# Performance work log

Measured on AMD Instinct MI355X. Metric: run time of the kernel, lower is better.

## Reference

```python
import jax, jax.numpy as jnp
import numpy as np

B, L, H = 4, 200, 225   # batch, seq_len, hidden (=15*15)
V = 221                 # input_dim + 1 (padding_idx=0)
EPS = 1e-5


def _bn(x, g, b):
    # training-mode batchnorm over (N, spatial), channel axis = 1
    red = (0,) + tuple(range(2, x.ndim))
    m = jnp.mean(x, red, keepdims=True)
    v = jnp.var(x, red, keepdims=True)
    shp = [1] * x.ndim
    shp[1] = -1
    return (x - m) / jnp.sqrt(v + EPS) * g.reshape(shp) + b.reshape(shp)


def _conv3(x, w, sd):
    return jax.lax.conv_general_dilated(
        x, w, (sd, 1, 1), [(1, 1)] * 3,
        dimension_numbers=('NCDHW', 'OIDHW', 'NCDHW'))


def _conv2(x, w):
    return jax.lax.conv_general_dilated(
        x, w, (1, 1), [(1, 1)] * 2,
        dimension_numbers=('NCHW', 'OIHW', 'NCHW'))


def setup_inputs():
    key = jax.random.key(0)
    ks = jax.random.split(key, 16)

    def he(k, shape, fan_in):
        return jax.random.normal(k, shape, jnp.float32) * (2.0 / fan_in) ** 0.5

    emb = he(ks[0], (V, H), H).at[0].set(0.0)  # padding_idx=0 row zeroed
    w3a = he(ks[1], (4, 1, 3, 3, 3), 1 * 27)
    w3b = he(ks[2], (8, 4, 3, 3, 3), 4 * 27)
    w3c = he(ks[3], (4, 8, 3, 3, 3), 8 * 27)
    w3d = he(ks[4], (1, 4, 3, 3, 3), 4 * 27)
    w2 = he(ks[5], (5, 25, 25, 3, 3), 25 * 9)  # 5 residual conv2d blocks
    fc1_w = he(ks[6], (200, 450), 450)
    fc1_b = jnp.zeros((200,), jnp.float32)
    fc2_w = he(ks[7], (1, 200), 200)
    fc2_b = jnp.zeros((1,), jnp.float32)
    x = jax.random.randint(ks[8], (B, L), 0, V)
    return dict(
        x=x, emb=emb,
        w3a=w3a, g3a=jnp.ones(4), b3a=jnp.zeros(4),
        w3b=w3b, g3b=jnp.ones(8), b3b=jnp.zeros(8),
        w3c=w3c, g3c=jnp.ones(4), b3c=jnp.zeros(4),
        w3d=w3d, g3d=jnp.ones(1), b3d=jnp.zeros(1),
        w2=w2, g2=jnp.ones((5, 25)), b2=jnp.zeros((5, 25)),
        fc1_w=fc1_w, fc1_b=fc1_b, fc2_w=fc2_w, fc2_b=fc2_b)


def reference(x, emb, w3a, g3a, b3a, w3b, g3b, b3b, w3c, g3c, b3c,
              w3d, g3d, b3d, w2, g2, b2, fc1_w, fc1_b, fc2_w, fc2_b):
    e = emb[x]                                  # [B,L,225]
    img = e.reshape(B, L, 15, 15)
    # vectorized replacement of python double-loop causal mask/pad construction:
    # c3d[b,i,t] = img[b,t] if t <= i else 0
    mask = jnp.tril(jnp.ones((L, L), e.dtype))
    c3d = (img[:, None] * mask[None, :, :, None, None]).reshape(B * L, 1, L, 15, 15)

    h = jax.nn.relu(_bn(_conv3(c3d, w3a, 1), g3a, b3a))   # [N,4,200,15,15]
    h = jax.nn.relu(_bn(_conv3(h, w3b, 2), g3b, b3b))     # [N,8,100,15,15]
    h = jax.nn.relu(_bn(_conv3(h, w3c, 2), g3c, b3c))     # [N,4,50,15,15]
    h = jax.nn.relu(_bn(_conv3(h, w3d, 2), g3d, b3d))     # [N,1,25,15,15]

    z = h[:, 0]                                 # squeeze -> [N,25,15,15]
    for i in range(5):
        z = z + jax.nn.relu(_bn(_conv2(z, w2[i]), g2[i], b2[i]))

    # AdaptiveAvgPool3d((1,15,15)) on [N,1,25,15,15] == mean over depth 25
    pooled = jnp.mean(z, axis=1).reshape(B * L, 225)
    feat = jnp.concatenate([pooled, e.reshape(B * L, 225)], axis=1)  # [N,450]
    hfc = jnp.tanh(feat @ fc1_w.T + fc1_b)
    return jax.nn.sigmoid(hfc @ fc2_w.T + fc2_b)  # [N,1]
```

## Files before the change

### kernel.cpp

```cpp
#include <hip/hip_runtime.h>
#include <math.h>

#define DEV __device__ __forceinline__

constexpr int B = 4, L = 200, SP = 225;
constexpr int C1 = 4, D1 = 200;
constexpr int C2N = 8, D2 = 100;
constexpr int C3N = 4, D3 = 50;
constexpr int D4 = 25;
constexpr float EPS = 1e-5f;

constexpr size_t OFF_F1  = 0;
constexpr size_t OFF_E2  = OFF_F1  + 720000;
constexpr size_t OFF_E1  = OFF_E2  + 720000;
constexpr size_t OFF_SS1 = OFF_E1  + 720000;
constexpr size_t OFF_PAR = OFF_SS1 + 19200;
constexpr size_t OFF_F2  = OFF_PAR + 1024;
constexpr size_t OFF_C2  = OFF_F2  + 720000;
constexpr size_t OFF_T2  = OFF_C2  + 1800;
constexpr size_t OFF_SS2F= OFF_T2  + 2880000;
constexpr size_t OFF_SS2T= OFF_SS2F+ 6400;
constexpr size_t OFF_SS2C= OFF_SS2T+ 51200;
constexpr size_t OFF_F3  = OFF_SS2C+ 16;
constexpr size_t OFF_C3  = OFF_F3  + 180000;
constexpr size_t OFF_T3  = OFF_C3  + 900;
constexpr size_t OFF_SS3F= OFF_T3  + 1440000;
constexpr size_t OFF_SS3T= OFF_SS3F+ 1600;
constexpr size_t OFF_SS3C= OFF_SS3T+ 12800;
constexpr size_t OFF_F4  = OFF_SS3C+ 8;
constexpr size_t OFF_C4  = OFF_F4  + 22500;
constexpr size_t OFF_T4  = OFF_C4  + 225;
constexpr size_t OFF_SS4F= OFF_T4  + 360000;
constexpr size_t OFF_SS4T= OFF_SS4F+ 200;
constexpr size_t OFF_SS4C= OFF_SS4T+ 3200;
constexpr size_t OFF_Z   = OFF_SS4C+ 2;
constexpr size_t OFF_CB  = OFF_Z   + 4500000;
constexpr size_t OFF_P2D = OFF_CB  + 4500000;
constexpr size_t WS_FLOATS = OFF_P2D + 40000;


DEV float waveRed(float v) {
    #pragma unroll
    for (int m = 32; m; m >>= 1) v += __shfl_xor(v, m, 64);
    return v;
}
DEV double blockSumD(double v, double* red) {
    int tid = threadIdx.x;
    red[tid] = v; __syncthreads();
    for (int s = 128; s > 0; s >>= 1) { if (tid < s) red[tid] += red[tid + s]; __syncthreads(); }
    double r = red[0]; __syncthreads(); return r;
}
DEV float conv9(const float* S, const float* w, int y, int x) {
    float a = 0.f;
    for (int ky = 0; ky < 3; ky++) { int yy = y + ky - 1; if (yy < 0 || yy >= 15) continue;
        for (int kx = 0; kx < 3; kx++) { int xx = x + kx - 1; if (xx < 0 || xx >= 15) continue;
            a += w[ky * 3 + kx] * S[yy * 15 + xx]; } }
    return a;
}
DEV void gather9(const float* Sp, int y, int x, float* s9) {
    #pragma unroll
    for (int ky = 0; ky < 3; ky++) {
        int yy = y + ky - 1; bool oky = (yy >= 0 && yy < 15);
        #pragma unroll
        for (int kx = 0; kx < 3; kx++) {
            int xx = x + kx - 1; bool ok = oky && (xx >= 0 && xx < 15);
            s9[ky * 3 + kx] = ok ? Sp[yy * 15 + xx] : 0.f;
        }
    }
}

__global__ __launch_bounds__(256) void k_layer1(const int* __restrict__ xi, const float* __restrict__ emb,
                        const float* __restrict__ w3a, float* F1, float* E2, float* E1, float* SS1) {
    __shared__ float simg[675];
    __shared__ float red[96];
    int blk = blockIdx.x;
    int d = blk % D1; int b = blk / D1;
    int tid = threadIdx.x;
    for (int idx = tid; idx < 675; idx += 256) {
        int t = idx / 225, pos = idx % 225;
        int j = d + t - 1; float v = 0.f;
        if (j >= 0 && j < L) v = emb[(size_t)xi[b * L + j] * SP + pos];
        simg[idx] = v;
    }
    __syncthreads();
    int y = tid / 15, x = tid % 15;
    int w = tid >> 6;
    #pragma unroll 1
    for (int c = 0; c < 4; c++) {
        float f1 = 0.f, e2 = 0.f, e1 = 0.f;
        if (tid < 225) {
            float P0 = conv9(simg,       w3a + c * 27,      y, x);
            float P1 = conv9(simg + 225, w3a + c * 27 + 9,  y, x);
            float P2 = conv9(simg + 450, w3a + c * 27 + 18, y, x);
            f1 = P0 + P1 + P2; e2 = P0 + P1; e1 = P0;
            size_t o = ((size_t)(b * C1 + c) * D1 + d) * SP + tid;
            F1[o] = f1; E2[o] = e2; E1[o] = e1;
        }
        float r0 = waveRed(f1), r1 = waveRed(f1 * f1), r2 = waveRed(e2),
              r3 = waveRed(e2 * e2), r4 = waveRed(e1), r5 = waveRed(e1 * e1);
        if ((tid & 63) == 0) {
            float* rp = red + w * 24 + c * 6;
            rp[0] = r0; rp[1] = r1; rp[2] = r2; rp[3] = r3; rp[4] = r4; rp[5] = r5;
        }
    }
    __syncthreads();
    if (tid < 24) {
        float s = red[tid] + red[24 + tid] + red[48 + tid] + red[72 + tid];
        int c = tid / 6, q = tid % 6;
        SS1[q * 3200 + (b * C1 + c) * D1 + d] = s;
    }
}

__global__ void k_stats1(const float* SS1, const float* g, const float* bb, float* par) {
    __shared__ double dred[256];
    int c = blockIdx.x; int tid = threadIdx.x;
    double s = 0, q = 0;
    for (int idx = tid; idx < B * D1; idx += 256) {
        int b = idx / D1, d = idx % D1;
        int sl = (b * C1 + c) * D1 + d;
        double wF = (double)(L - 1 - d);
        s += wF * SS1[sl] + SS1[6400 + sl] + (d >= 1 ? SS1[12800 + sl] : 0.0);
        q += wF * SS1[3200 + sl] + SS1[9600 + sl] + (d >= 1 ? SS1[16000 + sl] : 0.0);
    }
    s = blockSumD(s, dred); q = blockSumD(q, dred);
    if (tid == 0) {
        double N = (double)B * L * D1 * SP;
        double mean = s / N, var = q / N - mean * mean;
        float sc = g[c] / (float)sqrt(var + (double)EPS);
        float sh = bb[c] - (float)mean * sc;
        par[c] = sc; par[4 + c] = sh; par[8 + c] = fmaxf(sh, 0.f);
    }
}

__global__ __launch_bounds__(256) void k_F2(const float* __restrict__ F1raw, const float* __restrict__ par,
                        const float* __restrict__ w3b, float* F2, float* SS2F) {
    __shared__ float S[2700];
    __shared__ float red[8];
    int blk = blockIdx.x; int d2 = blk % D2; int c2 = (blk / D2) % C2N; int b = blk / (D2 * C2N);
    int tid = threadIdx.x;
    for (int idx = tid; idx < 2700; idx += 256) {
        int p = idx / 225, pos = idx % 225; int t = p >> 2, c = p & 3;
        int j = 2 * d2 - 1 + t; float v = 0.f;
        if (j >= 0 && j < D1)
            v = fmaxf(par[c] * F1raw[((size_t)(b * C1 + c) * D1 + j) * SP + pos] + par[4 + c], 0.f);
        S[idx] = v;
    }
    __syncthreads();
    float acc = 0.f;
    if (tid < 225) {
        int y = tid / 15, x = tid % 15;
        #pragma unroll 1
        for (int t = 0; t < 3; t++)
            for (int c = 0; c < 4; c++)
                acc += conv9(S + (t * 4 + c) * 225, w3b + c2 * 108 + c * 27 + t * 9, y, x);
        F2[(size_t)blk * SP + tid] = acc;
    }
    float sm = waveRed(acc), sq = waveRed(acc * acc);
    if ((tid & 63) == 0) { red[(tid >> 6) * 2] = sm; red[(tid >> 6) * 2 + 1] = sq; }
    __syncthreads();
    if (tid == 0) { SS2F[blk] = red[0] + red[2] + red[4] + red[6]; SS2F[3200 + blk] = red[1] + red[3] + red[5] + red[7]; }
}

__global__ void k_C2(const float* __restrict__ par, const float* __restrict__ w3b, float* C2b, float* SS2C) {
    __shared__ float red[64];
    int tid = threadIdx.x; int y = tid / 15, x = tid % 15; int w = tid >> 6;
    #pragma unroll 1
    for (int c2 = 0; c2 < C2N; c2++) {
        float acc = 0.f;
        if (tid < 225) {
            for (int c = 0; c < C1; c++) {
                float z1 = par[8 + c];
                for (int t = 0; t < 3; t++) {
                    float ws = 0.f;
                    for (int ky = 0; ky < 3; ky++) { int yy = y + ky - 1; if (yy < 0 || yy >= 15) continue;
                        for (int kx = 0; kx < 3; kx++) { int xx = x + kx - 1; if (xx < 0 || xx >= 15) continue;
                            ws += w3b[c2 * 108 + c * 27 + t * 9 + ky * 3 + kx]; } }
                    acc += z1 * ws;
                }
            }
            C2b[c2 * SP + tid] = acc;
        }
        float sm = waveRed(acc), sq = waveRed(acc * acc);
        if ((tid & 63) == 0) { red[w * 16 + c2 * 2] = sm; red[w * 16 + c2 * 2 + 1] = sq; }
    }
    __syncthreads();
    if (tid < 16) SS2C[tid] = red[tid] + red[16 + tid] + red[32 + tid] + red[48 + tid];
}

__global__ __launch_bounds__(512) void k_T2(const float* __restrict__ F1raw, const float* __restrict__ E2raw,
                    const float* __restrict__ E1raw, const float* __restrict__ par,
                    const float* __restrict__ w3b, float* T2, float* SS2T) {
    __shared__ float S[4500];
    __shared__ float red[128];
    int blk = blockIdx.x; int i = blk % L, b = blk / L; int tid = threadIdx.x;
    int t2a = i >> 1, jbase = 2 * t2a - 1;
    for (int idx = tid; idx < 4500; idx += 512) {
        int p = idx / 225, pos = idx % 225; int sl = p >> 2, c = p & 3;
        int j = jbase + sl; float v = 0.f;
        if (j >= 0 && j < L) {
            if (j <= i - 1)      v = fmaxf(par[c] * F1raw[((size_t)(b * C1 + c) * D1 + j) * SP + pos] + par[4 + c], 0.f);
            else if (j == i)     v = fmaxf(par[c] * E2raw[((size_t)(b * C1 + c) * D1 + j) * SP + pos] + par[4 + c], 0.f);
            else if (j == i + 1) v = fmaxf(par[c] * E1raw[((size_t)(b * C1 + c) * D1 + j) * SP + pos] + par[4 + c], 0.f);
            else                 v = par[8 + c];
        }
        S[idx] = v;
    }
    __syncthreads();
    int g = tid >> 8;
    int tp = tid & 255;
    int y = tp / 15, x = tp % 15;
    float vals[8] = {0,0,0,0,0,0,0,0};
    int d2 = t2a + g;
    if (d2 < D2 && tp < 225) {
        #pragma unroll 1
        for (int t = 0; t < 3; t++) {
            int sl = 2 * g + t;
            #pragma unroll 1
            for (int c = 0; c < 4; c++) {
                float s9[9];
                gather9(S + (sl * 4 + c) * 225, y, x, s9);
                const float* wb = w3b + c * 27 + t * 9;
                #pragma unroll
                for (int c2 = 0; c2 < 8; c2++) {
                    const float* wc = wb + c2 * 108;
                    float a = 0.f;
                    #pragma unroll
                    for (int q = 0; q < 9; q++) a += wc[q] * s9[q];
                    vals[c2] += a;
                }
            }
        }
    }
    if (tp < 225)
        #pragma unroll
        for (int c2 = 0; c2 < 8; c2++) T2[(((size_t)blk * 2 + g) * C2N + c2) * SP + tp] = vals[c2];
    int w = tid >> 6;
    #pragma unroll
    for (int c2 = 0; c2 < 8; c2++) {
        float sm = waveRed(tp < 225 ? vals[c2] : 0.f), sq = waveRed(tp < 225 ? vals[c2] * vals[c2] : 0.f);
        if ((tid & 63) == 0) { red[w * 16 + c2 * 2] = sm; red[w * 16 + c2 * 2 + 1] = sq; }
    }
    __syncthreads();
    if (tid < 32) {
        int k = tid >> 4, idx = tid & 15;
        int c2 = idx >> 1, q = idx & 1;
        int wb = k * 4;
        float s = red[(wb + 0) * 16 + idx] + red[(wb + 1) * 16 + idx]
                + red[(wb + 2) * 16 + idx] + red[(wb + 3) * 16 + idx];
        (q ? SS2T + 25600 : SS2T)[((size_t)blk * 2 + k) * C2N + c2] = s;
    }
}

__global__ void k_stats2(const float* SS2F, const float* SS2T, const float* SS2C,
                         const float* g, const float* bb, float* par) {
    __shared__ double dred[256];
    int c2 = blockIdx.x; int tid = threadIdx.x;
    double s = 0, q = 0;
    for (int idx = tid; idx < B * D2; idx += 256) {
        int d2 = idx % D2; int b = idx / D2;
        int wv = L - 2 * d2 - 2; if (wv < 0) wv = 0;
        int sl = (b * C2N + c2) * D2 + d2;
        s += (double)wv * SS2F[sl]; q += (double)wv * SS2F[3200 + sl];
    }
    for (int idx = tid; idx < B * L * 2; idx += 256) {
        int sl = idx * C2N + c2;
        s += SS2T[sl]; q += SS2T[25600 + sl];
    }
    {
        int cnt = 0;
        for (int i = tid; i < L; i += 256) { int v = D2 - (i >> 1) - 2; if (v > 0) cnt += v; }
        double wv = (double)cnt * B;
        s += wv * SS2C[c2 * 2]; q += wv * SS2C[c2 * 2 + 1];
    }
    s = blockSumD(s, dred); q = blockSumD(q, dred);
    if (tid == 0) {
        double N = (double)B * L * D2 * SP;
        double mean = s / N, var = q / N - mean * mean;
        float sc = g[c2] / (float)sqrt(var + (double)EPS);
        float sh = bb[c2] - (float)mean * sc;
        par[16 + c2] = sc; par[24 + c2] = sh;
    }
}

__global__ __launch_bounds__(256) void k_F3(const float* __restrict__ F2raw, const float* __restrict__ par,
                        const float* __restrict__ w3c, float* F3, float* SS3F) {
    __shared__ float S[5400];
    __shared__ float red[8];
    int blk = blockIdx.x; int d3 = blk % D3; int c3 = (blk / D3) % C3N; int b = blk / (D3 * C3N);
    int tid = threadIdx.x;
    for (int idx = tid; idx < 5400; idx += 256) {
        int p = idx / 225, pos = idx % 225; int t = p >> 3, c2 = p & 7;
        int j2 = 2 * d3 - 1 + t; float v = 0.f;
        if (j2 >= 0 && j2 < D2)
            v = fmaxf(par[16 + c2] * F2raw[((size_t)(b * C2N + c2) * D2 + j2) * SP + pos] + par[24 + c2], 0.f);
        S[idx] = v;
    }
    __syncthreads();
    float acc = 0.f;
    if (tid < 225) {
        int y = tid / 15, x = tid % 15;
        #pragma unroll 1
        for (int t = 0; t < 3; t++)
            for (int c2 = 0; c2 < 8; c2++)
                acc += conv9(S + (t * 8 + c2) * 225, w3c + c3 * 216 + c2 * 27 + t * 9, y, x);
        F3[(size_t)blk * SP + tid] = acc;
    }
    float sm = waveRed(acc), sq = waveRed(acc * acc);
    if ((tid & 63) == 0) { red[(tid >> 6) * 2] = sm; red[(tid >> 6) * 2 + 1] = sq; }
    __syncthreads();
    if (tid == 0) { SS3F[blk] = red[0] + red[2] + red[4] + red[6]; SS3F[800 + blk] = red[1] + red[3] + red[5] + red[7]; }
}

__global__ void k_C3(const float* __restrict__ C2braw, const float* __restrict__ par,
                     const float* __restrict__ w3c, float* C3b, float* SS3C) {
    __shared__ float S[1800];
    __shared__ float red[32];
    int tid = threadIdx.x; int w = tid >> 6;
    for (int idx = tid; idx < 1800; idx += 256) {
        int c2 = idx / 225;
        S[idx] = fmaxf(par[16 + c2] * C2braw[idx] + par[24 + c2], 0.f);
    }
    __syncthreads();
    int y = tid / 15, x = tid % 15;
    #pragma unroll 1
    for (int c3 = 0; c3 < C3N; c3++) {
        float acc = 0.f;
        if (tid < 225) {
            for (int t = 0; t < 3; t++)
                for (int c2 = 0; c2 < C2N; c2++)
                    acc += conv9(S + c2 * 225, w3c + c3 * 216 + c2 * 27 + t * 9, y, x);
            C3b[c3 * SP + tid] = acc;
        }
        float sm = waveRed(acc), sq = waveRed(acc * acc);
        if ((tid & 63) == 0) { red[w * 8 + c3 * 2] = sm; red[w * 8 + c3 * 2 + 1] = sq; }
    }
    __syncthreads();
    if (tid < 8) SS3C[tid] = red[tid] + red[8 + tid] + red[16 + tid] + red[24 + tid];
}

__global__ __launch_bounds__(512) void k_T3(const float* __restrict__ F2raw, const float* __restrict__ T2raw,
                    const float* __restrict__ C2braw, const float* __restrict__ par,
                    const float* __restrict__ w3c, float* T3, float* SS3T) {
    __shared__ float S[9000];
    __shared__ float red[64];
    int blk = blockIdx.x; int i = blk % L, b = blk / L; int tid = threadIdx.x;
    int t2a = i >> 1, t3a = i >> 2, j2base = 2 * t3a - 1;
    for (int idx = tid; idx < 9000; idx += 512) {
        int p = idx / 225, pos = idx % 225; int sl = p >> 3, c2 = p & 7;
        int j2 = j2base + sl; float v = 0.f;
        if (j2 >= 0 && j2 < D2) {
            float raw;
            if (j2 < t2a)           raw = F2raw[((size_t)(b * C2N + c2) * D2 + j2) * SP + pos];
            else if (j2 == t2a)     raw = T2raw[(((size_t)blk * 2 + 0) * C2N + c2) * SP + pos];
            else if (j2 == t2a + 1) raw = T2raw[(((size_t)blk * 2 + 1) * C2N + c2) * SP + pos];
            else                    raw = C2braw[c2 * SP + pos];
            v = fmaxf(par[16 + c2] * raw + par[24 + c2], 0.f);
        }
        S[idx] = v;
    }
    __syncthreads();
    int g = tid >> 8;
    int tp = tid & 255;
    int y = tp / 15, x = tp % 15;
    float vals[4] = {0, 0, 0, 0};
    int d3 = t3a + g;
    if (d3 < D3 && tp < 225) {
        #pragma unroll 1
        for (int t = 0; t < 3; t++) {
            int sl = 2 * g + t;
            #pragma unroll 1
            for (int c2 = 0; c2 < 8; c2++) {
                float s9[9];
                gather9(S + (sl * 8 + c2) * 225, y, x, s9);
                const float* wb = w3c + c2 * 27 + t * 9;
                #pragma unroll
                for (int c3 = 0; c3 < 4; c3++) {
                    const float* wc = wb + c3 * 216;
                    float a = 0.f;
                    #pragma unroll
                    for (int q = 0; q < 9; q++) a += wc[q] * s9[q];
                    vals[c3] += a;
                }
            }
        }
    }
    if (tp < 225)
        #pragma unroll
        for (int c3 = 0; c3 < 4; c3++) T3[(((size_t)blk * 2 + g) * C3N + c3) * SP + tp] = vals[c3];
    int w = tid >> 6;
    #pragma unroll
    for (int c3 = 0; c3 < 4; c3++) {
        float sm = waveRed(tp < 225 ? vals[c3] : 0.f), sq = waveRed(tp < 225 ? vals[c3] * vals[c3] : 0.f);
        if ((tid & 63) == 0) { red[w * 8 + c3 * 2] = sm; red[w * 8 + c3 * 2 + 1] = sq; }
    }
    __syncthreads();
    if (tid < 16) {
        int k = tid >> 3, idx = tid & 7;
        int c3 = idx >> 1, q = idx & 1;
        int wb = k * 4;
        float s = red[(wb + 0) * 8 + idx] + red[(wb + 1) * 8 + idx]
                + red[(wb + 2) * 8 + idx] + red[(wb + 3) * 8 + idx];
        (q ? SS3T + 6400 : SS3T)[((size_t)blk * 2 + k) * C3N + c3] = s;
    }
}

__global__ void k_stats3(const float* SS3F, const float* SS3T, const float* SS3C,
                         const float* g, const float* bb, float* par) {
    __shared__ double dred[256];
    int c3 = blockIdx.x; int tid = threadIdx.x;
    double s = 0, q = 0;
    for (int idx = tid; idx < B * D3; idx += 256) {
        int d3 = idx % D3; int b = idx / D3;
        int wv = L - 4 * d3 - 4; if (wv < 0) wv = 0;
        int sl = (b * C3N + c3) * D3 + d3;
        s += (double)wv * SS3F[sl]; q += (double)wv * SS3F[800 + sl];
    }
    for (int idx = tid; idx < B * L * 2; idx += 256) {
        int sl = idx * C3N + c3;
        s += SS3T[sl]; q += SS3T[6400 + sl];
    }
    {
        int cnt = 0;
        for (int i = tid; i < L; i += 256) { int v = D3 - (i >> 2) - 2; if (v > 0) cnt += v; }
        double wv = (double)cnt * B;
        s += wv * SS3C[c3 * 2]; q += wv * SS3C[c3 * 2 + 1];
    }
    s = blockSumD(s, dred); q = blockSumD(q, dred);
    if (tid == 0) {
        double N = (double)B * L * D3 * SP;
        double mean = s / N, var = q / N - mean * mean;
        float sc = g[c3] / (float)sqrt(var + (double)EPS);
        float sh = bb[c3] - (float)mean * sc;
        par[32 + c3] = sc; par[36 + c3] = sh;
    }
}

__global__ __launch_bounds__(256) void k_F4(const float* __restrict__ F3raw, const float* __restrict__ par,
                        const float* __restrict__ w3d, float* F4, float* SS4F) {
    __shared__ float S[2700];
    __shared__ float red[8];
    int blk = blockIdx.x; int d4 = blk % D4; int b = blk / D4; int tid = threadIdx.x;
    for (int idx = tid; idx < 2700; idx += 256) {
        int p = idx / 225, pos = idx % 225; int t = p >> 2, c3 = p & 3;
        int j3 = 2 * d4 - 1 + t; float v = 0.f;
        if (j3 >= 0 && j3 < D3)
            v = fmaxf(par[32 + c3] * F3raw[((size_t)(b * C3N + c3) * D3 + j3) * SP + pos] + par[36 + c3], 0.f);
        S[idx] = v;
    }
    __syncthreads();
    float acc = 0.f;
    if (tid < 225) {
        int y = tid / 15, x = tid % 15;
        #pragma unroll 1
        for (int t = 0; t < 3; t++)
            for (int c3 = 0; c3 < 4; c3++)
                acc += conv9(S + (t * 4 + c3) * 225, w3d + c3 * 27 + t * 9, y, x);
        F4[(size_t)blk * SP + tid] = acc;
    }
    float sm = waveRed(acc), sq = waveRed(acc * acc);
    if ((tid & 63) == 0) { red[(tid >> 6) * 2] = sm; red[(tid >> 6) * 2 + 1] = sq; }
    __syncthreads();
    if (tid == 0) { SS4F[blk] = red[0] + red[2] + red[4] + red[6]; SS4F[100 + blk] = red[1] + red[3] + red[5] + red[7]; }
}

__global__ void k_C4(const float* __restrict__ C3braw, const float* __restrict__ par,
                     const float* __restrict__ w3d, float* C4b, float* SS4C) {
    __shared__ float S[900];
    __shared__ float red[8];
    int tid = threadIdx.x;
    for (int idx = tid; idx < 900; idx += 256) {
        int c3 = idx / 225;
        S[idx] = fmaxf(par[32 + c3] * C3braw[idx] + par[36 + c3], 0.f);
    }
    __syncthreads();
    int y = tid / 15, x = tid % 15;
    float acc = 0.f;
    if (tid < 225) {
        for (int t = 0; t < 3; t++)
            for (int c3 = 0; c3 < C3N; c3++)
                acc += conv9(S + c3 * 225, w3d + c3 * 27 + t * 9, y, x);
        C4b[tid] = acc;
    }
    float sm = waveRed(acc), sq = waveRed(acc * acc);
    if ((tid & 63) == 0) { red[(tid >> 6) * 2] = sm; red[(tid >> 6) * 2 + 1] = sq; }
    __syncthreads();
    if (tid == 0) { SS4C[0] = red[0] + red[2] + red[4] + red[6]; SS4C[1] = red[1] + red[3] + red[5] + red[7]; }
}

__global__ __launch_bounds__(512) void k_T4(const float* __restrict__ F3raw, const float* __restrict__ T3raw,
                    const float* __restrict__ C3braw, const float* __restrict__ par,
                    const float* __restrict__ w3d, float* T4, float* SS4T) {
    __shared__ float S[4500];
    __shared__ float red[16];
    int blk = blockIdx.x; int i = blk % L, b = blk / L; int tid = threadIdx.x;
    int t3a = i >> 2, t4a = i >> 3, j3base = 2 * t4a - 1;
    for (int idx = tid; idx < 4500; idx += 512) {
        int p = idx / 225, pos = idx % 225; int sl = p >> 2, c3 = p & 3;
        int j3 = j3base + sl; float v = 0.f;
        if (j3 >= 0 && j3 < D3) {
            float raw;
            if (j3 < t3a)           raw = F3raw[((size_t)(b * C3N + c3) * D3 + j3) * SP + pos];
            else if (j3 == t3a)     raw = T3raw[(((size_t)blk * 2 + 0) * C3N + c3) * SP + pos];
            else if (j3 == t3a + 1) raw = T3raw[(((size_t)blk * 2 + 1) * C3N + c3) * SP + pos];
            else                    raw = C3braw[c3 * SP + pos];
            v = fmaxf(par[32 + c3] * raw + par[36 + c3], 0.f);
        }
        S[idx] = v;
    }
    __syncthreads();
    int g = tid >> 8;
    int tp = tid & 255;
    int y = tp / 15, x = tp % 15;
    float acc = 0.f;
    int d4 = t4a + g;
    if (d4 < D4 && tp < 225) {
        #pragma unroll 1
        for (int t = 0; t < 3; t++) {
            int sl = 2 * g + t;
            #pragma unroll 1
            for (int c3 = 0; c3 < 4; c3++) {
                float s9[9];
                gather9(S + (sl * 4 + c3) * 225, y, x, s9);
                const float* wc = w3d + c3 * 27 + t * 9;
                float a = 0.f;
                #pragma unroll
                for (int q = 0; q < 9; q++) a += wc[q] * s9[q];
                acc += a;
            }
        }
    }
    if (tp < 225) T4[((size_t)blk * 2 + g) * SP + tp] = acc;
    int w = tid >> 6;
    float sm = waveRed(tp < 225 ? acc : 0.f), sq = waveRed(tp < 225 ? acc * acc : 0.f);
    if ((tid & 63) == 0) { red[w * 2] = sm; red[w * 2 + 1] = sq; }
    __syncthreads();
    if (tid < 4) {
        int k = tid >> 1, q = tid & 1;
        int wb = k * 4;
        float s = red[(wb + 0) * 2 + q] + red[(wb + 1) * 2 + q] + red[(wb + 2) * 2 + q] + red[(wb + 3) * 2 + q];
        (q ? SS4T + 1600 : SS4T)[blk * 2 + k] = s;
    }
}

__global__ void k_stats4(const float* SS4F, const float* SS4T, const float* SS4C,
                         const float* g, const float* bb, float* par) {
    __shared__ double dred[256];
    int tid = threadIdx.x; double s = 0, q = 0;
    for (int idx = tid; idx < B * D4; idx += 256) {
        int d4 = idx % D4; int b = idx / D4;
        int wv = L - 8 * d4 - 8; if (wv < 0) wv = 0;
        s += (double)wv * SS4F[b * D4 + d4]; q += (double)wv * SS4F[100 + b * D4 + d4];
    }
    for (int idx = tid; idx < B * L * 2; idx += 256) {
        s += SS4T[idx]; q += SS4T[1600 + idx];
    }
    {
        int cnt = 0;
        for (int i = tid; i < L; i += 256) { int v = D4 - (i >> 3) - 2; if (v > 0) cnt += v; }
        double wv = (double)cnt * B;
        s += wv * SS4C[0]; q += wv * SS4C[1];
    }
    s = blockSumD(s, dred); q = blockSumD(q, dred);
    if (tid == 0) {
        double N = (double)B * L * D4 * SP;
        double mean = s / N, var = q / N - mean * mean;
        float sc = g[0] / (float)sqrt(var + (double)EPS);
        float sh = bb[0] - (float)mean * sc;
        par[40] = sc; par[41] = sh;
    }
}

__global__ void k_trfc1(const float* __restrict__ fc1w, float* __restrict__ fc1T) {
    int idx = blockIdx.x * 256 + threadIdx.x;
    if (idx >= 200 * 450) return;
    int o = idx % 200, k = idx / 200;
    fc1T[idx] = fc1w[(size_t)o * 450 + k];
}

template<int MODE>
__global__ __launch_bounds__(384) void k_conv2d(const float* __restrict__ zin, float* __restrict__ zout,
        const float* __restrict__ cprev, const float* __restrict__ par,
        const float* __restrict__ F4s, const float* __restrict__ T4s, const float* __restrict__ C4s,
        const float* __restrict__ w2it, float* __restrict__ cbuf, float* __restrict__ part) {
    __shared__ float zs[5625];
    __shared__ float rowsum[375], rowsq[375];
    int s = blockIdx.x, tid = threadIdx.x;
    int i = s % L, b = s / L; int t4a = i >> 3;
    for (int idx = tid; idx < 5625; idx += 384) {
        int c = idx / 225, pos = idx % 225;
        float v;
        if (MODE == 0) {
            float raw;
            if (c < t4a)           raw = F4s[((size_t)b * D4 + c) * SP + pos];
            else if (c == t4a)     raw = T4s[((size_t)s * 2 + 0) * SP + pos];
            else if (c == t4a + 1) raw = T4s[((size_t)s * 2 + 1) * SP + pos];
            else                   raw = C4s[pos];
            v = fmaxf(par[40] * raw + par[41], 0.f);
        } else {
            v = zin[(size_t)s * 5625 + idx] + fmaxf(par[48 + c] * cprev[(size_t)s * 5625 + idx] + par[80 + c], 0.f);
        }
        zout[(size_t)s * 5625 + idx] = v;
        zs[idx] = v;
    }
    __syncthreads();
    if (tid < 375) {
        int c2 = tid / 15, y = tid % 15;
        float acc[15];
        #pragma unroll
        for (int xx = 0; xx < 15; xx++) acc[xx] = 0.f;
        const float* wrow = w2it + c2 * 225;
        #pragma unroll 1
        for (int c = 0; c < 25; c++) {
            const float* wcc = wrow + c * 9;
            #pragma unroll
            for (int ky = 0; ky < 3; ky++) {
                int yy = y + ky - 1; if (yy < 0 || yy >= 15) continue;
                const float* zr = zs + c * 225 + yy * 15;
                float w0 = __ldg(wcc + ky * 3 + 0), w1 = __ldg(wcc + ky * 3 + 1), w2v = __ldg(wcc + ky * 3 + 2);
                float rv[15];
                #pragma unroll
                for (int xx = 0; xx < 15; xx++) rv[xx] = zr[xx];
                acc[0] += w1 * rv[0] + w2v * rv[1];
                #pragma unroll
                for (int xx = 1; xx < 14; xx++) acc[xx] += w0 * rv[xx - 1] + w1 * rv[xx] + w2v * rv[xx + 1];
                acc[14] += w0 * rv[13] + w1 * rv[14];
            }
        }
        float sm = 0.f, sq = 0.f;
        #pragma unroll
        for (int xx = 0; xx < 15; xx++) {
            float v = acc[xx]; sm += v; sq += v * v;
            cbuf[(size_t)s * 5625 + tid * 15 + xx] = v;
        }
        rowsum[tid] = sm; rowsq[tid] = sq;
    }
    __syncthreads();
    if (tid < 25) {
        float sm = 0.f, sq = 0.f;
        for (int r = tid * 15; r < tid * 15 + 15; r++) { sm += rowsum[r]; sq += rowsq[r]; }
        part[((size_t)s * 25 + tid) * 2] = sm; part[((size_t)s * 25 + tid) * 2 + 1] = sq;
    }
}

__global__ void k_stats2d(const float* part, const float* g, const float* bb, float* par) {
    __shared__ double dred[256];
    int c = blockIdx.x, tid = threadIdx.x;
    double s = 0, q = 0;
    for (int ss = tid; ss < B * L; ss += 256) { s += part[((size_t)ss * 25 + c) * 2]; q += part[((size_t)ss * 25 + c) * 2 + 1]; }
    s = blockSumD(s, dred); q = blockSumD(q, dred);
    if (tid == 0) {
        double N = (double)B * L * SP;
        double mean = s / N, var = q / N - mean * mean;
        float sc = g[c] / (float)sqrt(var + (double)EPS);
        float sh = bb[c] - (float)mean * sc;
        par[48 + c] = sc; par[80 + c] = sh;
    }
}

__global__ __launch_bounds__(256) void k_head(const float* __restrict__ z, const float* __restrict__ cbuf,
                      const float* __restrict__ par, const int* __restrict__ xi, const float* __restrict__ emb,
                      const float* __restrict__ fc1T, const float* __restrict__ fc1b,
                      const float* __restrict__ fc2w, const float* __restrict__ fc2b,
                      float* __restrict__ out) {
    __shared__ float feat[450];
    __shared__ float red[4];
    int s = blockIdx.x, tid = threadIdx.x;
    if (tid < 225) {
        float sm = 0.f;
        for (int c = 0; c < 25; c++) {
            size_t o = (size_t)s * 5625 + c * 225 + tid;
            sm += z[o] + fmaxf(par[48 + c] * cbuf[o] + par[80 + c], 0.f);
        }
        feat[tid] = sm * (1.f / 25.f);
        feat[225 + tid] = emb[(size_t)xi[s] * SP + tid];
    }
    __syncthreads();
    float hv = 0.f;
    {
        float acc = (tid < 200) ? fc1b[tid] : 0.f;
        for (int k = 0; k < 450; k++) {
            float wv = (tid < 200) ? fc1T[k * 200 + tid] : 0.f;
            acc += feat[k] * wv;
        }
        if (tid < 200) hv = tanhf(acc) * fc2w[tid];
    }
    float tot = waveRed(hv);
    if ((tid & 63) == 0) red[tid >> 6] = tot;
    __syncthreads();
    if (tid == 0) out[s] = 1.f / (1.f + expf(-(red[0] + red[1] + red[2] + red[3] + fc2b[0])));
}

extern "C" void kernel_launch(void* const* d_in, const int* in_sizes, int n_in,
                              void* d_out, int out_size, void* d_ws, size_t ws_size,
                              hipStream_t stream) {
    const int*   xi   = (const int*)d_in[0];
    const float* emb  = (const float*)d_in[1];
    const float* w3a  = (const float*)d_in[2];
    const float* g3a  = (const float*)d_in[3];
    const float* b3a  = (const float*)d_in[4];
    const float* w3b  = (const float*)d_in[5];
    const float* g3b  = (const float*)d_in[6];
    const float* b3b  = (const float*)d_in[7];
    const float* w3c  = (const float*)d_in[8];
    const float* g3c  = (const float*)d_in[9];
    const float* b3c  = (const float*)d_in[10];
    const float* w3d  = (const float*)d_in[11];
    const float* g3d  = (const float*)d_in[12];
    const float* b3d  = (const float*)d_in[13];
    const float* w2   = (const float*)d_in[14];
    const float* g2   = (const float*)d_in[15];
    const float* b2   = (const float*)d_in[16];
    const float* fc1w = (const float*)d_in[17];
    const float* fc1b = (const float*)d_in[18];
    const float* fc2w = (const float*)d_in[19];
    const float* fc2b = (const float*)d_in[20];
    float* ws = (float*)d_ws;
    float* out = (float*)d_out;
    if (ws_size < WS_FLOATS * sizeof(float)) return;

    float* F1  = ws + OFF_F1;   float* E2  = ws + OFF_E2;  float* E1  = ws + OFF_E1;
    float* SS1 = ws + OFF_SS1;  float* par = ws + OFF_PAR;
    float* F2  = ws + OFF_F2;   float* C2b = ws + OFF_C2;  float* T2  = ws + OFF_T2;
    float* SS2F= ws + OFF_SS2F; float* SS2T= ws + OFF_SS2T; float* SS2C= ws + OFF_SS2C;
    float* F3  = ws + OFF_F3;   float* C3b = ws + OFF_C3;  float* T3  = ws + OFF_T3;
    float* SS3F= ws + OFF_SS3F; float* SS3T= ws + OFF_SS3T; float* SS3C= ws + OFF_SS3C;
    float* F4  = ws + OFF_F4;   float* C4b = ws + OFF_C4;  float* T4  = ws + OFF_T4;
    float* SS4F= ws + OFF_SS4F; float* SS4T= ws + OFF_SS4T; float* SS4C= ws + OFF_SS4C;
    float* z   = ws + OFF_Z;    float* cb  = ws + OFF_CB;  float* p2d = ws + OFF_P2D;
    float* fc1T = ws + OFF_E2;

    k_layer1<<<B * D1, 256, 0, stream>>>(xi, emb, w3a, F1, E2, E1, SS1);
    k_stats1<<<4, 256, 0, stream>>>(SS1, g3a, b3a, par);
    k_F2<<<B * C2N * D2, 256, 0, stream>>>(F1, par, w3b, F2, SS2F);
    k_C2<<<1, 256, 0, stream>>>(par, w3b, C2b, SS2C);
    k_T2<<<B * L, 512, 0, stream>>>(F1, E2, E1, par, w3b, T2, SS2T);
    k_trfc1<<<(90000 + 255) / 256, 256, 0, stream>>>(fc1w, fc1T);
    k_stats2<<<8, 256, 0, stream>>>(SS2F, SS2T, SS2C, g3b, b3b, par);
    k_F3<<<B * C3N * D3, 256, 0, stream>>>(F2, par, w3c, F3, SS3F);
    k_C3<<<1, 256, 0, stream>>>(C2b, par, w3c, C3b, SS3C);
    k_T3<<<B * L, 512, 0, stream>>>(F2, T2, C2b, par, w3c, T3, SS3T);
    k_stats3<<<4, 256, 0, stream>>>(SS3F, SS3T, SS3C, g3c, b3c, par);
    k_F4<<<B * D4, 256, 0, stream>>>(F3, par, w3d, F4, SS4F);
    k_C4<<<1, 256, 0, stream>>>(C3b, par, w3d, C4b, SS4C);
    k_T4<<<B * L, 512, 0, stream>>>(F3, T3, C3b, par, w3d, T4, SS4T);
    k_stats4<<<1, 256, 0, stream>>>(SS4F, SS4T, SS4C, g3d, b3d, par);

    k_conv2d<0><<<B * L, 384, 0, stream>>>(z, z, cb, par, F4, T4, C4b, w2, cb, p2d);
    k_stats2d<<<25, 256, 0, stream>>>(p2d, g2, b2, par);
    for (int it = 1; it < 5; it++) {
        k_conv2d<1><<<B * L, 384, 0, stream>>>(z, z, cb, par, F4, T4, C4b, w2 + (size_t)it * 5625, cb, p2d);
        k_stats2d<<<25, 256, 0, stream>>>(p2d, g2 + it * 25, b2 + it * 25, par);
    }
    k_head<<<B * L, 256, 0, stream>>>(z, cb, par, xi, emb, fc1T, fc1b, fc2w, fc2b, out);
}
```

Measured before the change: 572.1 us.

## Fuse five residual conv2d blocks into one persistent cooperative kernel

Replaces the ten launches of per-iteration conv2d plus batchnorm-stats kernels with a single cooperative kernel. Each block keeps its sample's 25x15x15 activation resident in shared memory across all five residual iterations, and grid-wide syncs handle the batchnorm reductions. This removes the global-memory round trips for z and the conv buffer, plus the launch overhead. It requires all 800 blocks of 384 threads (~25 KB LDS each) to be co-resident, and falls back to the old path if the cooperative launch fails. Pooling is split out so the head kernel reads precomputed pooled features.

```diff
diff --git a/kernel.cpp b/kernel.cpp
--- a/kernel.cpp
+++ b/kernel.cpp
@@ -1,5 +1,8 @@
 #include <hip/hip_runtime.h>
+#include <hip/hip_cooperative_groups.h>
 #include <math.h>
+
+namespace cg = cooperative_groups;
 
 #define DEV __device__ __forceinline__
 
@@ -44,6 +47,11 @@
     for (int m = 32; m; m >>= 1) v += __shfl_xor(v, m, 64);
     return v;
 }
+DEV double waveRedD(double v) {
+    #pragma unroll
+    for (int m = 32; m; m >>= 1) v += __shfl_xor(v, m, 64);
+    return v;
+}
 DEV double blockSumD(double v, double* red) {
     int tid = threadIdx.x;
     red[tid] = v; __syncthreads();
@@ -577,6 +585,106 @@
     fc1T[idx] = fc1w[(size_t)o * 450 + k];
 }
 
+__global__ __launch_bounds__(384, 8) void k_loop2d(
+        const float* __restrict__ F4s, const float* __restrict__ T4s, const float* __restrict__ C4s,
+        float* __restrict__ par, const float* __restrict__ w2,
+        const float* __restrict__ g2, const float* __restrict__ b2,
+        float* __restrict__ part, float* __restrict__ pooled) {
+    cg::grid_group grid = cg::this_grid();
+    __shared__ float zs[5625];
+    __shared__ float rowsum[375], rowsq[375];
+    __shared__ double dredS[6], dredQ[6];
+    int s = blockIdx.x, tid = threadIdx.x;
+    int i = s % L, b = s / L; int t4a = i >> 3;
+    for (int idx = tid; idx < 5625; idx += 384) {
+        int c = idx / 225, pos = idx % 225;
+        float raw;
+        if (c < t4a)           raw = F4s[((size_t)b * D4 + c) * SP + pos];
+        else if (c == t4a)     raw = T4s[((size_t)s * 2 + 0) * SP + pos];
+        else if (c == t4a + 1) raw = T4s[((size_t)s * 2 + 1) * SP + pos];
+        else                   raw = C4s[pos];
+        zs[idx] = fmaxf(par[40] * raw + par[41], 0.f);
+    }
+    __syncthreads();
+    int c2 = tid / 15, y = tid % 15;
+    #pragma unroll 1
+    for (int it = 0; it < 5; it++) {
+        const float* w2it = w2 + (size_t)it * 5625;
+        float acc[15];
+        #pragma unroll
+        for (int xx = 0; xx < 15; xx++) acc[xx] = 0.f;
+        if (tid < 375) {
+            const float* wrow = w2it + c2 * 225;
+            #pragma unroll 1
+            for (int c = 0; c < 25; c++) {
+                const float* wcc = wrow + c * 9;
+                #pragma unroll
+                for (int ky = 0; ky < 3; ky++) {
+                    int yy = y + ky - 1; if (yy < 0 || yy >= 15) continue;
+                    const float* zr = zs + c * 225 + yy * 15;
+                    float w0 = __ldg(wcc + ky * 3 + 0), w1 = __ldg(wcc + ky * 3 + 1), w2v = __ldg(wcc + ky * 3 + 2);
+                    float rv[15];
+                    #pragma unroll
+                    for (int xx = 0; xx < 15; xx++) rv[xx] = zr[xx];
+                    acc[0] += w1 * rv[0] + w2v * rv[1];
+                    #pragma unroll
+                    for (int xx = 1; xx < 14; xx++) acc[xx] += w0 * rv[xx - 1] + w1 * rv[xx] + w2v * rv[xx + 1];
+                    acc[14] += w0 * rv[13] + w1 * rv[14];
+                }
+            }
+            float sm = 0.f, sq = 0.f;
+            #pragma unroll
+            for (int xx = 0; xx < 15; xx++) { float v = acc[xx]; sm += v; sq += v * v; }
+            rowsum[tid] = sm; rowsq[tid] = sq;
+        }
+        __syncthreads();
+        if (tid < 25) {
+            float sm = 0.f, sq = 0.f;
+            for (int r = tid * 15; r < tid * 15 + 15; r++) { sm += rowsum[r]; sq += rowsq[r]; }
+            part[((size_t)s * 25 + tid) * 2] = sm; part[((size_t)s * 25 + tid) * 2 + 1] = sq;
+        }
+        __threadfence();
+        grid.sync();
+        if (blockIdx.x < 25) {
+            int c = blockIdx.x;
+            double sd = 0, qd = 0;
+            for (int ss = tid; ss < B * L; ss += 384) {
+                sd += part[((size_t)ss * 25 + c) * 2];
+                qd += part[((size_t)ss * 25 + c) * 2 + 1];
+            }
+            sd = waveRedD(sd); qd = waveRedD(qd);
+            if ((tid & 63) == 0) { dredS[tid >> 6] = sd; dredQ[tid >> 6] = qd; }
+            __syncthreads();
+            if (tid == 0) {
+                double S = 0, Q = 0;
+                for (int u = 0; u < 6; u++) { S += dredS[u]; Q += dredQ[u]; }
+                double N = (double)B * L * SP;
+                double mean = S / N, var = Q / N - mean * mean;
+                float sc = g2[it * 25 + c] / (float)sqrt(var + (double)EPS);
+                float sh = b2[it * 25 + c] - (float)mean * sc;
+                par[48 + c] = sc; par[80 + c] = sh;
+            }
+            __syncthreads();
+        }
+        __threadfence();
+        grid.sync();
+        if (tid < 375) {
+            float sc = par[48 + c2], sh = par[80 + c2];
+            float* zrow = zs + c2 * 225 + y * 15;
+            #pragma unroll
+            for (int xx = 0; xx < 15; xx++)
+                zrow[xx] += fmaxf(sc * acc[xx] + sh, 0.f);
+        }
+        __syncthreads();
+    }
+    if (tid < 225) {
+        float sm = 0.f;
+        #pragma unroll 1
+        for (int c = 0; c < 25; c++) sm += zs[c * 225 + tid];
+        pooled[(size_t)s * 225 + tid] = sm * (1.f / 25.f);
+    }
+}
+
 template<int MODE>
 __global__ __launch_bounds__(384) void k_conv2d(const float* __restrict__ zin, float* __restrict__ zout,
         const float* __restrict__ cprev, const float* __restrict__ par,
@@ -657,8 +765,21 @@
     }
 }
 
-__global__ __launch_bounds__(256) void k_head(const float* __restrict__ z, const float* __restrict__ cbuf,
-                      const float* __restrict__ par, const int* __restrict__ xi, const float* __restrict__ emb,
+__global__ __launch_bounds__(256) void k_pool(const float* __restrict__ z, const float* __restrict__ cbuf,
+                      const float* __restrict__ par, float* __restrict__ pooled) {
+    int s = blockIdx.x, tid = threadIdx.x;
+    if (tid < 225) {
+        float sm = 0.f;
+        for (int c = 0; c < 25; c++) {
+            size_t o = (size_t)s * 5625 + c * 225 + tid;
+            sm += z[o] + fmaxf(par[48 + c] * cbuf[o] + par[80 + c], 0.f);
+        }
+        pooled[(size_t)s * 225 + tid] = sm * (1.f / 25.f);
+    }
+}
+
+__global__ __launch_bounds__(256) void k_head(const float* __restrict__ pooled,
+                      const int* __restrict__ xi, const float* __restrict__ emb,
                       const float* __restrict__ fc1T, const float* __restrict__ fc1b,
                       const float* __restrict__ fc2w, const float* __restrict__ fc2b,
                       float* __restrict__ out) {
@@ -666,12 +787,7 @@
     __shared__ float red[4];
     int s = blockIdx.x, tid = threadIdx.x;
     if (tid < 225) {
-        float sm = 0.f;
-        for (int c = 0; c < 25; c++) {
-            size_t o = (size_t)s * 5625 + c * 225 + tid;
-            sm += z[o] + fmaxf(par[48 + c] * cbuf[o] + par[80 + c], 0.f);
-        }
-        feat[tid] = sm * (1.f / 25.f);
+        feat[tid] = pooled[(size_t)s * 225 + tid];
         feat[225 + tid] = emb[(size_t)xi[s] * SP + tid];
     }
     __syncthreads();
@@ -727,7 +843,8 @@
     float* F4  = ws + OFF_F4;   float* C4b = ws + OFF_C4;  float* T4  = ws + OFF_T4;
     float* SS4F= ws + OFF_SS4F; float* SS4T= ws + OFF_SS4T; float* SS4C= ws + OFF_SS4C;
     float* z   = ws + OFF_Z;    float* cb  = ws + OFF_CB;  float* p2d = ws + OFF_P2D;
-    float* fc1T = ws + OFF_E2;
+    float* fc1T   = ws + OFF_E2;
+    float* pooled = ws + OFF_E1;
 
     k_layer1<<<B * D1, 256, 0, stream>>>(xi, emb, w3a, F1, E2, E1, SS1);
     k_stats1<<<4, 256, 0, stream>>>(SS1, g3a, b3a, par);
@@ -745,11 +862,23 @@
     k_T4<<<B * L, 512, 0, stream>>>(F3, T3, C3b, par, w3d, T4, SS4T);
     k_stats4<<<1, 256, 0, stream>>>(SS4F, SS4T, SS4C, g3d, b3d, par);
 
-    k_conv2d<0><<<B * L, 384, 0, stream>>>(z, z, cb, par, F4, T4, C4b, w2, cb, p2d);
-    k_stats2d<<<25, 256, 0, stream>>>(p2d, g2, b2, par);
-    for (int it = 1; it < 5; it++) {
-        k_conv2d<1><<<B * L, 384, 0, stream>>>(z, z, cb, par, F4, T4, C4b, w2 + (size_t)it * 5625, cb, p2d);
-        k_stats2d<<<25, 256, 0, stream>>>(p2d, g2 + it * 25, b2 + it * 25, par);
-    }
-    k_head<<<B * L, 256, 0, stream>>>(z, cb, par, xi, emb, fc1T, fc1b, fc2w, fc2b, out);
-}
+    hipError_t coopErr;
+    {
+        const float* F4c = F4; const float* T4c = T4; const float* C4c = C4b;
+        const float* w2c = w2; const float* g2c = g2; const float* b2c = b2;
+        float* parc = par; float* partc = p2d; float* pooledc = pooled;
+        void* args[] = { (void*)&F4c, (void*)&T4c, (void*)&C4c, (void*)&parc,
+                         (void*)&w2c, (void*)&g2c, (void*)&b2c, (void*)&partc, (void*)&pooledc };
+        coopErr = hipLaunchCooperativeKernel((const void*)k_loop2d, dim3(B * L), dim3(384), args, 0, stream);
+    }
+    if (coopErr != hipSuccess) {
+        k_conv2d<0><<<B * L, 384, 0, stream>>>(z, z, cb, par, F4, T4, C4b, w2, cb, p2d);
+        k_stats2d<<<25, 256, 0, stream>>>(p2d, g2, b2, par);
+        for (int it = 1; it < 5; it++) {
+            k_conv2d<1><<<B * L, 384, 0, stream>>>(z, z, cb, par, F4, T4, C4b, w2 + (size_t)it * 5625, cb, p2d);
+            k_stats2d<<<25, 256, 0, stream>>>(p2d, g2 + it * 25, b2 + it * 25, par);
+        }
+        k_pool<<<B * L, 256, 0, stream>>>(z, cb, par, pooled);
+    }
+    k_head<<<B * L, 256, 0, stream>>>(pooled, xi, emb, fc1T, fc1b, fc2w, fc2b, out);
+}
```

Measured after the change: 2.238 ms. 291% more time.

## Split residual conv2d channels across two blocks with ping-pong z buffers

Applied to the files above, without the earlier changes.

Adds a conv2d variant that launches two blocks per sample, each computing about half the output channels (13 each, with channel 12 computed by both). This doubles block-level parallelism for the five residual conv layers. Because the second half-block reads the previous z while the first half-block writes the updated one, z and the conv buffers are double-buffered in extra workspace. Each block still rebuilds the full 25-channel input tile, so global reads of the input roughly double. The new path runs only when the workspace is large enough; otherwise the original kernel is used.

```diff
diff --git a/kernel.cpp b/kernel.cpp
--- a/kernel.cpp
+++ b/kernel.cpp
@@ -37,6 +37,9 @@
 constexpr size_t OFF_CB  = OFF_Z   + 4500000;
 constexpr size_t OFF_P2D = OFF_CB  + 4500000;
 constexpr size_t WS_FLOATS = OFF_P2D + 40000;
+constexpr size_t OFF_Z1  = WS_FLOATS;
+constexpr size_t OFF_CB1 = OFF_Z1 + 4500000;
+constexpr size_t WS_PP   = OFF_CB1 + 4500000;
 
 
 DEV float waveRed(float v) {
@@ -639,6 +642,76 @@
         float sm = 0.f, sq = 0.f;
         for (int r = tid * 15; r < tid * 15 + 15; r++) { sm += rowsum[r]; sq += rowsq[r]; }
         part[((size_t)s * 25 + tid) * 2] = sm; part[((size_t)s * 25 + tid) * 2 + 1] = sq;
+    }
+}
+
+template<int MODE>
+__global__ __launch_bounds__(256) void k_conv2dPP(const float* __restrict__ zin, float* __restrict__ zout,
+        const float* __restrict__ cprev, const float* __restrict__ par,
+        const float* __restrict__ F4s, const float* __restrict__ T4s, const float* __restrict__ C4s,
+        const float* __restrict__ w2it, float* __restrict__ cbnext, float* __restrict__ part) {
+    __shared__ float zs[5625];
+    __shared__ float rowsum[195], rowsq[195];
+    int blk = blockIdx.x, tid = threadIdx.x;
+    int half = (blk >= 800) ? 1 : 0;
+    int s = blk - half * 800;
+    int c2base = half * 12;
+    int i = s % L, b = s / L; int t4a = i >> 3;
+    for (int idx = tid; idx < 5625; idx += 256) {
+        int c = idx / 225, pos = idx % 225;
+        float v;
+        if (MODE == 0) {
+            float raw;
+            if (c < t4a)           raw = F4s[((size_t)b * D4 + c) * SP + pos];
+            else if (c == t4a)     raw = T4s[((size_t)s * 2 + 0) * SP + pos];
+            else if (c == t4a + 1) raw = T4s[((size_t)s * 2 + 1) * SP + pos];
+            else                   raw = C4s[pos];
+            v = fmaxf(par[40] * raw + par[41], 0.f);
+        } else {
+            v = zin[(size_t)s * 5625 + idx] + fmaxf(par[48 + c] * cprev[(size_t)s * 5625 + idx] + par[80 + c], 0.f);
+        }
+        if (half == 0) zout[(size_t)s * 5625 + idx] = v;
+        zs[idx] = v;
+    }
+    __syncthreads();
+    if (tid < 195) {
+        int c2l = tid / 15, y = tid % 15;
+        int c2 = c2base + c2l;
+        float acc[15];
+        #pragma unroll
+        for (int xx = 0; xx < 15; xx++) acc[xx] = 0.f;
+        const float* wrow = w2it + c2 * 225;
+        #pragma unroll 1
+        for (int c = 0; c < 25; c++) {
+            const float* wcc = wrow + c * 9;
+            #pragma unroll
+            for (int ky = 0; ky < 3; ky++) {
+                int yy = y + ky - 1; if (yy < 0 || yy >= 15) continue;
+                const float* zr = zs + c * 225 + yy * 15;
+                float w0 = __ldg(wcc + ky * 3 + 0), w1 = __ldg(wcc + ky * 3 + 1), w2v = __ldg(wcc + ky * 3 + 2);
+                float rv[15];
+                #pragma unroll
+                for (int xx = 0; xx < 15; xx++) rv[xx] = zr[xx];
+                acc[0] += w1 * rv[0] + w2v * rv[1];
+                #pragma unroll
+                for (int xx = 1; xx < 14; xx++) acc[xx] += w0 * rv[xx - 1] + w1 * rv[xx] + w2v * rv[xx + 1];
+                acc[14] += w0 * rv[13] + w1 * rv[14];
+            }
+        }
+        float sm = 0.f, sq = 0.f;
+        #pragma unroll
+        for (int xx = 0; xx < 15; xx++) {
+            float v = acc[xx]; sm += v; sq += v * v;
+            cbnext[(size_t)s * 5625 + c2 * 225 + y * 15 + xx] = v;
+        }
+        rowsum[tid] = sm; rowsq[tid] = sq;
+    }
+    __syncthreads();
+    if (tid < 13) {
+        float sm = 0.f, sq = 0.f;
+        for (int r = tid * 15; r < tid * 15 + 15; r++) { sm += rowsum[r]; sq += rowsq[r]; }
+        int c2 = c2base + tid;
+        part[((size_t)s * 25 + c2) * 2] = sm; part[((size_t)s * 25 + c2) * 2 + 1] = sq;
     }
 }
 
@@ -728,6 +801,9 @@
     float* SS4F= ws + OFF_SS4F; float* SS4T= ws + OFF_SS4T; float* SS4C= ws + OFF_SS4C;
     float* z   = ws + OFF_Z;    float* cb  = ws + OFF_CB;  float* p2d = ws + OFF_P2D;
     float* fc1T = ws + OFF_E2;
+    bool pp = (ws_size >= WS_PP * sizeof(float));
+    float* zb[2]  = { z,  pp ? ws + OFF_Z1  : z };
+    float* cbb[2] = { cb, pp ? ws + OFF_CB1 : cb };
 
     k_layer1<<<B * D1, 256, 0, stream>>>(xi, emb, w3a, F1, E2, E1, SS1);
     k_stats1<<<4, 256, 0, stream>>>(SS1, g3a, b3a, par);
@@ -745,11 +821,22 @@
     k_T4<<<B * L, 512, 0, stream>>>(F3, T3, C3b, par, w3d, T4, SS4T);
     k_stats4<<<1, 256, 0, stream>>>(SS4F, SS4T, SS4C, g3d, b3d, par);
 
-    k_conv2d<0><<<B * L, 384, 0, stream>>>(z, z, cb, par, F4, T4, C4b, w2, cb, p2d);
-    k_stats2d<<<25, 256, 0, stream>>>(p2d, g2, b2, par);
-    for (int it = 1; it < 5; it++) {
-        k_conv2d<1><<<B * L, 384, 0, stream>>>(z, z, cb, par, F4, T4, C4b, w2 + (size_t)it * 5625, cb, p2d);
-        k_stats2d<<<25, 256, 0, stream>>>(p2d, g2 + it * 25, b2 + it * 25, par);
-    }
-    k_head<<<B * L, 256, 0, stream>>>(z, cb, par, xi, emb, fc1T, fc1b, fc2w, fc2b, out);
-}
+    if (pp) {
+        k_conv2dPP<0><<<1600, 256, 0, stream>>>(nullptr, zb[0], nullptr, par, F4, T4, C4b, w2, cbb[0], p2d);
+        k_stats2d<<<25, 256, 0, stream>>>(p2d, g2, b2, par);
+        for (int it = 1; it < 5; it++) {
+            k_conv2dPP<1><<<1600, 256, 0, stream>>>(zb[(it - 1) & 1], zb[it & 1], cbb[(it - 1) & 1], par,
+                                                    F4, T4, C4b, w2 + (size_t)it * 5625, cbb[it & 1], p2d);
+            k_stats2d<<<25, 256, 0, stream>>>(p2d, g2 + it * 25, b2 + it * 25, par);
+        }
+        k_head<<<B * L, 256, 0, stream>>>(zb[0], cbb[0], par, xi, emb, fc1T, fc1b, fc2w, fc2b, out);
+    } else {
+        k_conv2d<0><<<B * L, 384, 0, stream>>>(z, z, cb, par, F4, T4, C4b, w2, cb, p2d);
+        k_stats2d<<<25, 256, 0, stream>>>(p2d, g2, b2, par);
+        for (int it = 1; it < 5; it++) {
+            k_conv2d<1><<<B * L, 384, 0, stream>>>(z, z, cb, par, F4, T4, C4b, w2 + (size_t)it * 5625, cb, p2d);
+            k_stats2d<<<25, 256, 0, stream>>>(p2d, g2 + it * 25, b2 + it * 25, par);
+        }
+        k_head<<<B * L, 256, 0, stream>>>(z, cb, par, xi, emb, fc1T, fc1b, fc2w, fc2b, out);
+    }
+}
```

After: 600.2 us. 4.9% more time.
